# Optimization experiments

Measured on AMD Instinct MI355X. Metric: run time of the kernel, lower is better.

## Reference

```python
import jax, jax.numpy as jnp
import numpy as np

N = 50000        # nodes
E = 250000       # edges (first N are self-loops -> every node has in-degree >= 1)
H = 12           # num_heads
D = 64           # per-head dim (in_dim == out_dim == 64)
NEG_SLOPE = 0.2  # LeakyReLU alpha


def setup_inputs() -> dict:
    key = jax.random.key(0)
    k1, k2, k3, k4, k5, k6, k7 = jax.random.split(key, 7)
    h = jax.random.normal(k1, (N, H * D), dtype=jnp.float32)
    # self-loops + random in-neighbors so segment softmax is well defined for all dst
    src = jnp.concatenate([jnp.arange(N, dtype=jnp.int32),
                           jax.random.randint(k2, (E - N,), 0, N, dtype=jnp.int32)])
    dst = jnp.concatenate([jnp.arange(N, dtype=jnp.int32),
                           jax.random.randint(k3, (E - N,), 0, N, dtype=jnp.int32)])
    xav = 1.414 / np.sqrt(D)  # ~ xavier_normal gain=1.414
    W_fc = jax.random.normal(k4, (D, D), dtype=jnp.float32) * xav
    attn_l = jax.random.normal(k5, (H, D), dtype=jnp.float32) * 0.15
    attn_r = jax.random.normal(k6, (H, D), dtype=jnp.float32) * 0.15
    W_res = jax.random.normal(k7, (D, D), dtype=jnp.float32) * xav
    return {"h": h, "W_fc": W_fc, "attn_l": attn_l, "attn_r": attn_r,
            "W_res": W_res, "src": src, "dst": dst}


def reference(h, W_fc, attn_l, attn_r, W_res, src, dst):
    n = h.shape[0]
    hh = h.reshape(n, H, D)                              # [N,H,D]
    # fc is Linear(D, D, bias=False) shared across heads: y = x @ W^T
    ft = jnp.einsum('nhd,ed->nhe', hh, W_fc)             # [N,H,D]
    a1 = jnp.einsum('nhd,hd->nh', ft, attn_l)            # [N,H]
    a2 = jnp.einsum('nhd,hd->nh', ft, attn_r)            # [N,H]
    # edge_attention: leaky_relu(src.a1 + dst.a2)
    e = jax.nn.leaky_relu(a1[src] + a2[dst], negative_slope=NEG_SLOPE)  # [E,H]
    # segment softmax over incoming edges per destination node (stable)
    m = jax.ops.segment_max(e, dst, num_segments=n)       # [N,H]
    ee = jnp.exp(e - m[dst])                              # [E,H]
    denom = jax.ops.segment_sum(ee, dst, num_segments=n)  # [N,H]
    alpha = ee / denom[dst]                               # [E,H]
    # message: alpha * src ft, scatter-sum into dst
    agg = jax.ops.segment_sum(alpha[:, :, None] * ft[src], dst, num_segments=n)  # [N,H,D]
    # residual: res_fc(h) per head, then ReLU(flatten)
    res = jnp.einsum('nhd,ed->nhe', hh, W_res)            # [N,H,D]
    return jax.nn.relu((res + agg).reshape(n, H * D))     # [N,768]
```

## Files before the change

### kernel.cpp

```cpp
#include <hip/hip_runtime.h>
#include <hip/hip_bf16.h>

#define N_NODES 50000
#define N_EDGES 250000
#define NHEAD   12
#define NH      (N_NODES * NHEAD)
#define ROW_TILES (NH / 16)
#define NGEMMB  1954
#define NFILLB  977

typedef __bf16 bf16_t;
typedef __bf16 bf16x8 __attribute__((ext_vector_type(8)));
typedef __bf16 bf16x4 __attribute__((ext_vector_type(4)));
typedef float  f32x4  __attribute__((ext_vector_type(4)));

__device__ __forceinline__ bf16x8 cvt8(f32x4 a, f32x4 b) {
    bf16x8 r;
    r[0] = (bf16_t)a[0]; r[1] = (bf16_t)a[1]; r[2] = (bf16_t)a[2]; r[3] = (bf16_t)a[3];
    r[4] = (bf16_t)b[0]; r[5] = (bf16_t)b[1]; r[6] = (bf16_t)b[2]; r[7] = (bf16_t)b[3];
    return r;
}

__device__ __forceinline__ uint2 pack4(f32x4 z) {
    bf16x4 p;
    p[0] = (bf16_t)z[0]; p[1] = (bf16_t)z[1]; p[2] = (bf16_t)z[2]; p[3] = (bf16_t)z[3];
    union { bf16x4 b; uint2 u; } c; c.b = p;
    return c.u;
}

__device__ __forceinline__ void xpose4(uint2 c0, uint2 c1, uint2 c2, uint2 c3,
                                       int lr, int lg,
                                       uint2& g0, uint2& g1, uint2& g2, uint2& g3) {
    g0 = g1 = g2 = g3 = make_uint2(0, 0);
#pragma unroll
    for (int k = 0; k < 4; ++k) {
        int sel = (lg - k) & 3;
        uint2 P = (sel == 0) ? c0 : (sel == 1) ? c1 : (sel == 2) ? c2 : c3;
        int srcl = lr + 16 * ((lg + k) & 3);
        uint2 R;
        R.x = (unsigned)__shfl((int)P.x, srcl, 64);
        R.y = (unsigned)__shfl((int)P.y, srcl, 64);
        int m = (lg + k) & 3;
        g0 = (m == 0) ? R : g0;
        g1 = (m == 1) ? R : g1;
        g2 = (m == 2) ? R : g2;
        g3 = (m == 3) ? R : g3;
    }
}

__global__ __launch_bounds__(256) void k_deg_prep(
    const int* __restrict__ dst, int* __restrict__ deg,
    const float* __restrict__ wfc, const float* __restrict__ wres,
    const float* __restrict__ attl, const float* __restrict__ attr,
    bf16_t* __restrict__ wfb, bf16_t* __restrict__ wrb,
    bf16_t* __restrict__ ulb, bf16_t* __restrict__ urb)
{
    int b = blockIdx.x;
    if (b < 245) {
        int i4 = b * 256 + threadIdx.x;
        if (i4 < N_EDGES / 4) {
            int4 q = reinterpret_cast<const int4*>(dst)[i4];
            atomicAdd(&deg[q.x], 1);
            atomicAdd(&deg[q.y], 1);
            atomicAdd(&deg[q.z], 1);
            atomicAdd(&deg[q.w], 1);
        }
    } else if (b < 261) {
        int t = (b - 245) * 256 + threadIdx.x;
        wfb[t] = (bf16_t)wfc[t];
        wrb[t] = (bf16_t)wres[t];
    } else if (b < 265) {
        int u = (b - 261) * 256 + threadIdx.x;
        int hh = u >> 6, d = u & 63;
        float s = 0.f;
        if (hh < NHEAD) {
#pragma unroll 8
            for (int e = 0; e < 64; ++e) s += attl[hh * 64 + e] * wfc[e * 64 + d];
        }
        ulb[u] = (bf16_t)s;
    } else {
        int u = (b - 265) * 256 + threadIdx.x;
        int hh = u >> 6, d = u & 63;
        float s = 0.f;
        if (hh < NHEAD) {
#pragma unroll 8
            for (int e = 0; e < 64; ++e) s += attr[hh * 64 + e] * wfc[e * 64 + d];
        }
        urb[u] = (bf16_t)s;
    }
}

__global__ __launch_bounds__(1024) void k_scan(const int* __restrict__ deg,
                                               int* __restrict__ cursor) {
    __shared__ int s[1024];
    const int CH = 52;
    int t = threadIdx.x;
    int base = t * CH;
    int loc[CH];
    if (base + CH <= N_NODES) {
        const int4* p = reinterpret_cast<const int4*>(deg + base);
#pragma unroll
        for (int i = 0; i < CH / 4; ++i) {
            int4 q = p[i];
            loc[4 * i + 0] = q.x; loc[4 * i + 1] = q.y;
            loc[4 * i + 2] = q.z; loc[4 * i + 3] = q.w;
        }
    } else {
#pragma unroll
        for (int i = 0; i < CH; ++i) {
            int idx = base + i;
            loc[i] = (idx < N_NODES) ? deg[idx] : 0;
        }
    }
    int sum = 0;
#pragma unroll
    for (int i = 0; i < CH; ++i) sum += loc[i];
    s[t] = sum;
    __syncthreads();
    for (int off = 1; off < 1024; off <<= 1) {
        int v = (t >= off) ? s[t - off] : 0;
        __syncthreads();
        s[t] += v;
        __syncthreads();
    }
    int run = s[t] - sum;
#pragma unroll
    for (int i = 0; i < CH; ++i) {
        int idx = base + i;
        if (idx < N_NODES) {
            cursor[idx] = run;
            run += loc[i];
        }
    }
}

__global__ __launch_bounds__(256) void k_fill_gemm(
    const int* __restrict__ src, const int* __restrict__ dst,
    int* __restrict__ cursor, int* __restrict__ csr_src,
    const float* __restrict__ h,
    const bf16_t* __restrict__ wfb,
    const bf16_t* __restrict__ wrb,
    const bf16_t* __restrict__ ulb,
    const bf16_t* __restrict__ urb,
    bf16_t* __restrict__ ft,
    bf16_t* __restrict__ resb,
    float* __restrict__ al,
    float* __restrict__ ar)
{
    int bid = blockIdx.x;
    if (bid % 3 == 2) {
        int i = (bid / 3) * 256 + threadIdx.x;
        if (i < N_EDGES) {
            int d = dst[i];
            int pos = atomicAdd(&cursor[d], 1);
            csr_src[pos] = src[i];
        }
        return;
    }
    int gid  = (bid / 3) * 2 + (bid % 3);
    int wv   = threadIdx.x >> 6;
    int lane = threadIdx.x & 63;
    int lr = lane & 15, lg = lane >> 4;

    const f32x4*  hv  = reinterpret_cast<const f32x4*>(h);
    const bf16x8* wf  = reinterpret_cast<const bf16x8*>(wfb);
    const bf16x8* wr  = reinterpret_cast<const bf16x8*>(wrb);
    const bf16x8* ulv = reinterpret_cast<const bf16x8*>(ulb);
    const bf16x8* urv = reinterpret_cast<const bf16x8*>(urb);
    bf16x8 ul0 = ulv[lr * 8 + lg], ul1 = ulv[lr * 8 + 4 + lg];
    bf16x8 ur0 = urv[lr * 8 + lg], ur1 = urv[lr * 8 + 4 + lg];

    const int nw = NGEMMB * 4;
    int tile = gid * 4 + wv;

    f32x4 c0, c1, c2, c3;
    if (tile < ROW_TILES) {
        int ab = (tile * 16 + lr) * 16 + lg * 2;
        c0 = __builtin_nontemporal_load(hv + ab);
        c1 = __builtin_nontemporal_load(hv + ab + 1);
        c2 = __builtin_nontemporal_load(hv + ab + 8);
        c3 = __builtin_nontemporal_load(hv + ab + 9);
    }
    while (tile < ROW_TILES) {
        int nxt = tile + nw;
        f32x4 n0, n1, n2, n3;
        if (nxt < ROW_TILES) {
            int ab = (nxt * 16 + lr) * 16 + lg * 2;
            n0 = __builtin_nontemporal_load(hv + ab);
            n1 = __builtin_nontemporal_load(hv + ab + 1);
            n2 = __builtin_nontemporal_load(hv + ab + 8);
            n3 = __builtin_nontemporal_load(hv + ab + 9);
        }
        bf16x8 a0 = cvt8(c0, c1), a1 = cvt8(c2, c3);
        int r0 = tile << 4;
        int r  = r0 + lr;
        int hh = r % NHEAD;

        f32x4 dl = {0.f, 0.f, 0.f, 0.f}, dr = {0.f, 0.f, 0.f, 0.f};
        dl = __builtin_amdgcn_mfma_f32_16x16x32_bf16(ul0, a0, dl, 0, 0, 0);
        dl = __builtin_amdgcn_mfma_f32_16x16x32_bf16(ul1, a1, dl, 0, 0, 0);
        dr = __builtin_amdgcn_mfma_f32_16x16x32_bf16(ur0, a0, dr, 0, 0, 0);
        dr = __builtin_amdgcn_mfma_f32_16x16x32_bf16(ur1, a1, dr, 0, 0, 0);
        if (lg == (hh >> 2)) {
#pragma unroll
            for (int j = 0; j < 4; ++j)
                if ((hh & 3) == j) { al[r] = dl[j]; ar[r] = dr[j]; }
        }

        uint2 pf[4], pe[4];
#pragma unroll
        for (int nt = 0; nt < 4; ++nt) {
            int brow = (nt * 16 + lr) * 8;
            f32x4 z = {0.f, 0.f, 0.f, 0.f};
            z = __builtin_amdgcn_mfma_f32_16x16x32_bf16(wf[brow + lg],     a0, z, 0, 0, 0);
            z = __builtin_amdgcn_mfma_f32_16x16x32_bf16(wf[brow + 4 + lg], a1, z, 0, 0, 0);
            f32x4 y = {0.f, 0.f, 0.f, 0.f};
            y = __builtin_amdgcn_mfma_f32_16x16x32_bf16(wr[brow + lg],     a0, y, 0, 0, 0);
            y = __builtin_amdgcn_mfma_f32_16x16x32_bf16(wr[brow + 4 + lg], a1, y, 0, 0, 0);
            pf[nt] = pack4(z);
            pe[nt] = pack4(y);
        }

        uint2 f0, f1, f2, f3, e0, e1, e2, e3;
        xpose4(pf[0], pf[1], pf[2], pf[3], lr, lg, f0, f1, f2, f3);
        xpose4(pe[0], pe[1], pe[2], pe[3], lr, lg, e0, e1, e2, e3);
        uint4 flo = make_uint4(f0.x, f0.y, f1.x, f1.y);
        uint4 fhi = make_uint4(f2.x, f2.y, f3.x, f3.y);
        uint4 elo = make_uint4(e0.x, e0.y, e1.x, e1.y);
        uint4 ehi = make_uint4(e2.x, e2.y, e3.x, e3.y);
        *reinterpret_cast<uint4*>(ft   + r * 64 + lg * 16)     = flo;
        *reinterpret_cast<uint4*>(ft   + r * 64 + lg * 16 + 8) = fhi;
        *reinterpret_cast<uint4*>(resb + r * 64 + lg * 16)     = elo;
        *reinterpret_cast<uint4*>(resb + r * 64 + lg * 16 + 8) = ehi;

        c0 = n0; c1 = n1; c2 = n2; c3 = n3;
        tile = nxt;
    }
}

#define DB 8
__global__ __launch_bounds__(256) void k_agg(
    const int* __restrict__ cur, const int* __restrict__ csr_src,
    const float* __restrict__ al, const float* __restrict__ ar,
    const bf16_t* __restrict__ ft, const bf16_t* __restrict__ resb,
    float* __restrict__ out)
{
    int d0 = (blockIdx.x * 256 + threadIdx.x) >> 6;
    d0 = __builtin_amdgcn_readfirstlane(d0);
    if (d0 >= N_NODES) return;
    int l  = threadIdx.x & 63;
    int hA = l >> 3;
    int hB = 8 + (l >> 4);
    int u_l = l / 12;
    int h_l = l - u_l * 12;
    int beg = d0 ? cur[d0 - 1] : 0;
    int end = cur[d0];
    float arW = 0.f;
    if (l < 48) arW = ar[d0 * NHEAD + h_l];

    float accA[8] = {0,0,0,0,0,0,0,0};
    float accB[4] = {0,0,0,0};
    float denA = 0.f, denB = 0.f;

    for (int j0 = beg; j0 < end; j0 += DB) {
        int idx[DB];
#pragma unroll
        for (int u = 0; u < DB; ++u) {
            int j = j0 + u;
            idx[u] = csr_src[(j < end) ? j : beg];
        }
        float wv0 = 0.f, wv1 = 0.f;
        {
            int e0 = idx[0], e1 = idx[4];
            e0 = (u_l == 1) ? idx[1] : e0;  e1 = (u_l == 1) ? idx[5] : e1;
            e0 = (u_l == 2) ? idx[2] : e0;  e1 = (u_l == 2) ? idx[6] : e1;
            e0 = (u_l == 3) ? idx[3] : e0;  e1 = (u_l == 3) ? idx[7] : e1;
            if (l < 48) {
                float x0 = al[e0 * NHEAD + h_l] + arW;
                float x1 = al[e1 * NHEAD + h_l] + arW;
                x0 = (x0 > 0.f) ? x0 : 0.2f * x0;
                x1 = (x1 > 0.f) ? x1 : 0.2f * x1;
                wv0 = ((j0 + u_l)     < end) ? __expf(x0) : 0.f;
                wv1 = ((j0 + 4 + u_l) < end) ? __expf(x1) : 0.f;
            }
        }
        float wA[DB], wB[DB];
#pragma unroll
        for (int u = 0; u < 4; ++u) {
            wA[u]     = __shfl(wv0, u * 12 + hA, 64);
            wB[u]     = __shfl(wv0, u * 12 + hB, 64);
            wA[u + 4] = __shfl(wv1, u * 12 + hA, 64);
            wB[u + 4] = __shfl(wv1, u * 12 + hB, 64);
        }
        bf16x8 vA[DB]; bf16x4 vB[DB];
#pragma unroll
        for (int u = 0; u < DB; ++u) {
            const bf16_t* row = ft + idx[u] * 768;
            vA[u] = *reinterpret_cast<const bf16x8*>(row + 8 * l);
            vB[u] = *reinterpret_cast<const bf16x4*>(row + 512 + 4 * l);
        }
#pragma unroll
        for (int u = 0; u < DB; ++u) {
            denA += wA[u]; denB += wB[u];
#pragma unroll
            for (int k = 0; k < 8; ++k) accA[k] += wA[u] * (float)vA[u][k];
#pragma unroll
            for (int k = 0; k < 4; ++k) accB[k] += wB[u] * (float)vB[u][k];
        }
    }

    const bf16_t* rrow = resb + d0 * 768;
    bf16x8 rA = __builtin_nontemporal_load(reinterpret_cast<const bf16x8*>(rrow + 8 * l));
    bf16x4 rB = __builtin_nontemporal_load(reinterpret_cast<const bf16x4*>(rrow + 512 + 4 * l));
    float* orow = out + d0 * 768;
    f32x4 o0, o1, o2;
    float ia = 1.f / denA, ib = 1.f / denB;
#pragma unroll
    for (int k = 0; k < 4; ++k) {
        float x = (float)rA[k] + accA[k] * ia;         o0[k] = x > 0.f ? x : 0.f;
        float y = (float)rA[k + 4] + accA[k + 4] * ia; o1[k] = y > 0.f ? y : 0.f;
        float z = (float)rB[k] + accB[k] * ib;         o2[k] = z > 0.f ? z : 0.f;
    }
    __builtin_nontemporal_store(o0, reinterpret_cast<f32x4*>(orow + 8 * l));
    __builtin_nontemporal_store(o1, reinterpret_cast<f32x4*>(orow + 8 * l + 4));
    __builtin_nontemporal_store(o2, reinterpret_cast<f32x4*>(orow + 512 + 4 * l));
}

extern "C" void kernel_launch(void* const* d_in, const int* in_sizes, int n_in,
                              void* d_out, int out_size, void* d_ws, size_t ws_size,
                              hipStream_t stream) {
    const float* h    = (const float*)d_in[0];
    const float* wfc  = (const float*)d_in[1];
    const float* attl = (const float*)d_in[2];
    const float* attr = (const float*)d_in[3];
    const float* wres = (const float*)d_in[4];
    const int*   src  = (const int*)d_in[5];
    const int*   dst  = (const int*)d_in[6];
    float* out = (float*)d_out;

    char* ws = (char*)d_ws;
    bf16_t* ft     = (bf16_t*)(ws + 0);
    bf16_t* resb   = (bf16_t*)(ws + 76800000);
    float*  al     = (float*)(ws + 153600000);
    float*  ar     = (float*)(ws + 156000000);
    int*    deg    = (int*)(ws + 158400000);
    int*    cursor = (int*)(ws + 158800896);
    int*    csrsrc = (int*)(ws + 159001344);
    bf16_t* wfb    = (bf16_t*)(ws + 160001344);
    bf16_t* wrb    = (bf16_t*)(ws + 160009536);
    bf16_t* ulb    = (bf16_t*)(ws + 160017728);
    bf16_t* urb    = (bf16_t*)(ws + 160019776);

    (void)hipMemsetAsync(deg, 0, N_NODES * sizeof(int), stream);
    k_deg_prep<<<269, 256, 0, stream>>>(dst, deg, wfc, wres, attl, attr, wfb, wrb, ulb, urb);
    k_scan<<<1, 1024, 0, stream>>>(deg, cursor);
    k_fill_gemm<<<NGEMMB + NFILLB, 256, 0, stream>>>(src, dst, cursor, csrsrc,
                                                     h, wfb, wrb, ulb, urb, ft, resb, al, ar);
    k_agg<<<(N_NODES + 3) / 4, 256, 0, stream>>>(cursor, csrsrc, al, ar, ft, resb, out);
}
```

Baseline: 223.2 us.

## Unroll GEMM tile loop with two-deep prefetch and separate fill blocks

Replaces the GEMM tile while-loop with a fully unrolled sequence of at most four tiles per wave. Two tiles' worth of input loads are kept in flight, so global loads overlap with the MFMA work. The GEMM block count is raised so four strides cover all row tiles. The CSR fill blocks are moved from an interleaved every-third-block pattern to a contiguous range after the GEMM blocks. That reduces how much the atomics overlap with GEMM blocks, and the extra live registers may lower occupancy.

```diff
diff --git a/kernel.cpp b/kernel.cpp
--- a/kernel.cpp
+++ b/kernel.cpp
@@ -6,7 +6,7 @@
 #define NHEAD   12
 #define NH      (N_NODES * NHEAD)
 #define ROW_TILES (NH / 16)
-#define NGEMMB  1954
+#define NGEMMB  2344
 #define NFILLB  977
 
 typedef __bf16 bf16_t;
@@ -134,6 +134,53 @@
     }
 }
 
+#define LOAD_A(B0, B1, B2, B3, T) {                                   \
+    int ab_ = ((T) * 16 + lr) * 16 + lg * 2;                          \
+    B0 = __builtin_nontemporal_load(hv + ab_);                        \
+    B1 = __builtin_nontemporal_load(hv + ab_ + 1);                    \
+    B2 = __builtin_nontemporal_load(hv + ab_ + 8);                    \
+    B3 = __builtin_nontemporal_load(hv + ab_ + 9); }
+
+#define COMP_T(B0, B1, B2, B3, TILE) {                                              \
+    bf16x8 a0_ = cvt8(B0, B1), a1_ = cvt8(B2, B3);                                  \
+    int r0_ = (TILE) << 4;                                                          \
+    int r_  = r0_ + lr;                                                             \
+    int hh_ = r_ % NHEAD;                                                           \
+    f32x4 dl_ = {0.f,0.f,0.f,0.f}, dr_ = {0.f,0.f,0.f,0.f};                         \
+    dl_ = __builtin_amdgcn_mfma_f32_16x16x32_bf16(ul0, a0_, dl_, 0, 0, 0);          \
+    dl_ = __builtin_amdgcn_mfma_f32_16x16x32_bf16(ul1, a1_, dl_, 0, 0, 0);          \
+    dr_ = __builtin_amdgcn_mfma_f32_16x16x32_bf16(ur0, a0_, dr_, 0, 0, 0);          \
+    dr_ = __builtin_amdgcn_mfma_f32_16x16x32_bf16(ur1, a1_, dr_, 0, 0, 0);          \
+    if (lg == (hh_ >> 2)) {                                                         \
+        _Pragma("unroll")                                                           \
+        for (int j = 0; j < 4; ++j)                                                 \
+            if ((hh_ & 3) == j) { al[r_] = dl_[j]; ar[r_] = dr_[j]; }               \
+    }                                                                               \
+    uint2 pf_[4], pe_[4];                                                           \
+    _Pragma("unroll")                                                               \
+    for (int nt = 0; nt < 4; ++nt) {                                                \
+        int brow_ = (nt * 16 + lr) * 8;                                             \
+        f32x4 z_ = {0.f,0.f,0.f,0.f};                                               \
+        z_ = __builtin_amdgcn_mfma_f32_16x16x32_bf16(wf[brow_ + lg],     a0_, z_, 0, 0, 0); \
+        z_ = __builtin_amdgcn_mfma_f32_16x16x32_bf16(wf[brow_ + 4 + lg], a1_, z_, 0, 0, 0); \
+        f32x4 y_ = {0.f,0.f,0.f,0.f};                                               \
+        y_ = __builtin_amdgcn_mfma_f32_16x16x32_bf16(wr[brow_ + lg],     a0_, y_, 0, 0, 0); \
+        y_ = __builtin_amdgcn_mfma_f32_16x16x32_bf16(wr[brow_ + 4 + lg], a1_, y_, 0, 0, 0); \
+        pf_[nt] = pack4(z_);                                                        \
+        pe_[nt] = pack4(y_);                                                        \
+    }                                                                               \
+    uint2 f0_, f1_, f2_, f3_, e0_, e1_, e2_, e3_;                                   \
+    xpose4(pf_[0], pf_[1], pf_[2], pf_[3], lr, lg, f0_, f1_, f2_, f3_);             \
+    xpose4(pe_[0], pe_[1], pe_[2], pe_[3], lr, lg, e0_, e1_, e2_, e3_);             \
+    uint4 flo_ = make_uint4(f0_.x, f0_.y, f1_.x, f1_.y);                            \
+    uint4 fhi_ = make_uint4(f2_.x, f2_.y, f3_.x, f3_.y);                            \
+    uint4 elo_ = make_uint4(e0_.x, e0_.y, e1_.x, e1_.y);                            \
+    uint4 ehi_ = make_uint4(e2_.x, e2_.y, e3_.x, e3_.y);                            \
+    *reinterpret_cast<uint4*>(ft   + r_ * 64 + lg * 16)     = flo_;                 \
+    *reinterpret_cast<uint4*>(ft   + r_ * 64 + lg * 16 + 8) = fhi_;                 \
+    *reinterpret_cast<uint4*>(resb + r_ * 64 + lg * 16)     = elo_;                 \
+    *reinterpret_cast<uint4*>(resb + r_ * 64 + lg * 16 + 8) = ehi_; }
+
 __global__ __launch_bounds__(256) void k_fill_gemm(
     const int* __restrict__ src, const int* __restrict__ dst,
     int* __restrict__ cursor, int* __restrict__ csr_src,
@@ -148,8 +195,8 @@
     float* __restrict__ ar)
 {
     int bid = blockIdx.x;
-    if (bid % 3 == 2) {
-        int i = (bid / 3) * 256 + threadIdx.x;
+    if (bid >= NGEMMB) {
+        int i = (bid - NGEMMB) * 256 + threadIdx.x;
         if (i < N_EDGES) {
             int d = dst[i];
             int pos = atomicAdd(&cursor[d], 1);
@@ -157,7 +204,6 @@
         }
         return;
     }
-    int gid  = (bid / 3) * 2 + (bid % 3);
     int wv   = threadIdx.x >> 6;
     int lane = threadIdx.x & 63;
     int lr = lane & 15, lg = lane >> 4;
@@ -171,71 +217,22 @@
     bf16x8 ur0 = urv[lr * 8 + lg], ur1 = urv[lr * 8 + 4 + lg];
 
     const int nw = NGEMMB * 4;
-    int tile = gid * 4 + wv;
-
-    f32x4 c0, c1, c2, c3;
-    if (tile < ROW_TILES) {
-        int ab = (tile * 16 + lr) * 16 + lg * 2;
-        c0 = __builtin_nontemporal_load(hv + ab);
-        c1 = __builtin_nontemporal_load(hv + ab + 1);
-        c2 = __builtin_nontemporal_load(hv + ab + 8);
-        c3 = __builtin_nontemporal_load(hv + ab + 9);
-    }
-    while (tile < ROW_TILES) {
-        int nxt = tile + nw;
-        f32x4 n0, n1, n2, n3;
-        if (nxt < ROW_TILES) {
-            int ab = (nxt * 16 + lr) * 16 + lg * 2;
-            n0 = __builtin_nontemporal_load(hv + ab);
-            n1 = __builtin_nontemporal_load(hv + ab + 1);
-            n2 = __builtin_nontemporal_load(hv + ab + 8);
-            n3 = __builtin_nontemporal_load(hv + ab + 9);
-        }
-        bf16x8 a0 = cvt8(c0, c1), a1 = cvt8(c2, c3);
-        int r0 = tile << 4;
-        int r  = r0 + lr;
-        int hh = r % NHEAD;
-
-        f32x4 dl = {0.f, 0.f, 0.f, 0.f}, dr = {0.f, 0.f, 0.f, 0.f};
-        dl = __builtin_amdgcn_mfma_f32_16x16x32_bf16(ul0, a0, dl, 0, 0, 0);
-        dl = __builtin_amdgcn_mfma_f32_16x16x32_bf16(ul1, a1, dl, 0, 0, 0);
-        dr = __builtin_amdgcn_mfma_f32_16x16x32_bf16(ur0, a0, dr, 0, 0, 0);
-        dr = __builtin_amdgcn_mfma_f32_16x16x32_bf16(ur1, a1, dr, 0, 0, 0);
-        if (lg == (hh >> 2)) {
-#pragma unroll
-            for (int j = 0; j < 4; ++j)
-                if ((hh & 3) == j) { al[r] = dl[j]; ar[r] = dr[j]; }
-        }
-
-        uint2 pf[4], pe[4];
-#pragma unroll
-        for (int nt = 0; nt < 4; ++nt) {
-            int brow = (nt * 16 + lr) * 8;
-            f32x4 z = {0.f, 0.f, 0.f, 0.f};
-            z = __builtin_amdgcn_mfma_f32_16x16x32_bf16(wf[brow + lg],     a0, z, 0, 0, 0);
-            z = __builtin_amdgcn_mfma_f32_16x16x32_bf16(wf[brow + 4 + lg], a1, z, 0, 0, 0);
-            f32x4 y = {0.f, 0.f, 0.f, 0.f};
-            y = __builtin_amdgcn_mfma_f32_16x16x32_bf16(wr[brow + lg],     a0, y, 0, 0, 0);
-            y = __builtin_amdgcn_mfma_f32_16x16x32_bf16(wr[brow + 4 + lg], a1, y, 0, 0, 0);
-            pf[nt] = pack4(z);
-            pe[nt] = pack4(y);
-        }
-
-        uint2 f0, f1, f2, f3, e0, e1, e2, e3;
-        xpose4(pf[0], pf[1], pf[2], pf[3], lr, lg, f0, f1, f2, f3);
-        xpose4(pe[0], pe[1], pe[2], pe[3], lr, lg, e0, e1, e2, e3);
-        uint4 flo = make_uint4(f0.x, f0.y, f1.x, f1.y);
-        uint4 fhi = make_uint4(f2.x, f2.y, f3.x, f3.y);
-        uint4 elo = make_uint4(e0.x, e0.y, e1.x, e1.y);
-        uint4 ehi = make_uint4(e2.x, e2.y, e3.x, e3.y);
-        *reinterpret_cast<uint4*>(ft   + r * 64 + lg * 16)     = flo;
-        *reinterpret_cast<uint4*>(ft   + r * 64 + lg * 16 + 8) = fhi;
-        *reinterpret_cast<uint4*>(resb + r * 64 + lg * 16)     = elo;
-        *reinterpret_cast<uint4*>(resb + r * 64 + lg * 16 + 8) = ehi;
-
-        c0 = n0; c1 = n1; c2 = n2; c3 = n3;
-        tile = nxt;
-    }
+    int t0 = bid * 4 + wv;
+    int t1 = t0 + nw, t2 = t0 + 2 * nw, t3 = t0 + 3 * nw;
+    bool v0 = t0 < ROW_TILES, v1 = t1 < ROW_TILES,
+         v2 = t2 < ROW_TILES, v3 = t3 < ROW_TILES;
+
+    f32x4 A0, A1, A2, A3;
+    f32x4 B0, B1, B2, B3;
+
+    if (v0) LOAD_A(A0, A1, A2, A3, t0);
+    if (v1) LOAD_A(B0, B1, B2, B3, t1);
+    if (v0) COMP_T(A0, A1, A2, A3, t0);
+    if (v2) LOAD_A(A0, A1, A2, A3, t2);
+    if (v1) COMP_T(B0, B1, B2, B3, t1);
+    if (v3) LOAD_A(B0, B1, B2, B3, t3);
+    if (v2) COMP_T(A0, A1, A2, A3, t2);
+    if (v3) COMP_T(B0, B1, B2, B3, t3);
 }
 
 #define DB 8
```

Result: slower. 265.6 us (+19.0%).
